# Kernel optimization log

Hardware: AMD Instinct MI355X
Metric: run time of the kernel (lower is better)

## Reference

```python
import jax, jax.numpy as jnp
import numpy as np

BLOCK_SIZE = 1024
DILATIONS = (1, 2, 4, 8)


def setup_inputs() -> dict:
    key = jax.random.key(0)
    kq, kk, kv, kw, kb = jax.random.split(key, 5)
    b, h, L, hd = 4, 8, 4096, 64
    hidden = h * hd
    return {
        "query_states": jax.random.normal(kq, (b, h, L, hd), jnp.float32),
        "key_states": jax.random.normal(kk, (b, h, L, hd), jnp.float32),
        "value_states": jax.random.normal(kv, (b, h, L, hd), jnp.float32),
        "Wo": jax.random.normal(kw, (hidden, hidden), jnp.float32),
        "bo": jax.random.normal(kb, (hidden,), jnp.float32),
    }


def _dilated_branch(q, k, v, d):
    """One dilation pass: strided gather -> block attention.
    Returns de (bsz, nh, Ld, 1) detached exp-row-sums and a (bsz, nh, Ld, hd)."""
    b, h, L, hd = q.shape
    qs, ks, vs = q[:, :, ::d], k[:, :, ::d], v[:, :, ::d]
    Ld = qs.shape[2]
    bs = min(BLOCK_SIZE, Ld)          # torch.split: one short block if Ld < block_size
    nb = Ld // bs                      # even split for chosen q_len
    blk = lambda x: x.reshape(b, h, nb, bs, hd)
    qb, kb, vb = blk(qs), blk(ks), blk(vs)
    scores = jnp.einsum('bhnqd,bhnkd->bhnqk', qb, kb) / jnp.sqrt(jnp.float32(hd))
    # detached, unstabilized exp-sum (matches attn_weights.detach().exp().sum(-1))
    de = jax.lax.stop_gradient(jnp.exp(scores).sum(-1, keepdims=True)).reshape(b, h, Ld, 1)
    probs = jax.nn.softmax(scores.astype(jnp.float32), axis=-1).astype(q.dtype)
    a = jnp.einsum('bhnqk,bhnkd->bhnqd', probs, vb).reshape(b, h, Ld, hd)
    return de, a


def reference(query_states, key_states, value_states, Wo, bo):
    b, h, L, hd = query_states.shape
    w = jnp.zeros((b, h, L, 1), jnp.float32)
    des, rs = [], []
    for d in DILATIONS:
        de, a = _dilated_branch(query_states, key_states, value_states, d)
        des.append(de)
        rs.append(a)
        w = w.at[:, :, ::d].add(de)
    out = jnp.zeros_like(query_states)
    for d, de, a in zip(DILATIONS, des, rs):
        aw = de / w[:, :, ::d]                     # (b, h, Ld, 1) relative weight
        out = out.at[:, :, ::d].add((aw * a).astype(query_states.dtype))
    out = out.transpose(0, 2, 1, 3).reshape(b, L, h * hd)
    return out @ Wo.T + bo
```

## Files before the change

kernel.cpp:

```cpp
#include <hip/hip_runtime.h>
#include <hip/hip_bf16.h>

typedef __attribute__((ext_vector_type(8))) short bf16x8;
typedef __attribute__((ext_vector_type(4))) float f32x4;
typedef unsigned short u16;

union F8 { bf16x8 v; unsigned u[4]; u16 s[8]; uint4 q; };

__device__ __forceinline__ unsigned pk2(float a, float b) {
    __hip_bfloat162 t = __float22bfloat162_rn(make_float2(a, b));
    unsigned r; __builtin_memcpy(&r, &t, 4); return r;
}
__device__ __forceinline__ u16 f2bf(float a) {
    __hip_bfloat16 t = __float2bfloat16(a);
    u16 r; __builtin_memcpy(&r, &t, 2); return r;
}
__device__ __forceinline__ float bf2f(u16 s) {
    unsigned u = ((unsigned)s) << 16; float f; __builtin_memcpy(&f, &u, 4); return f;
}
#define SWZ(byteoff, row) ((byteoff) ^ (((row) & 7) << 4))
#define MFMA(a, b, c) __builtin_amdgcn_mfma_f32_16x16x32_bf16((a), (b), (c), 0, 0, 0)

__global__ __launch_bounds__(256)
void prep_kernel(const float* __restrict__ K, const float* __restrict__ V,
                 u16* __restrict__ Kb, u16* __restrict__ Vt)
{
    __shared__ __align__(16) char tl[64 * 128];
    int blk = blockIdx.x;
    const int t = threadIdx.x;

    if (blk < 2048) {
        const int bh = blk >> 6, qt = blk & 63;
        const int q = qt * 64 + (t >> 2), dd0 = (t & 3) * 16;
        const float* kp = K + ((size_t)bh * 4096 + q) * 64 + dd0;
        float4 x0 = ((const float4*)kp)[0], x1 = ((const float4*)kp)[1];
        float4 x2 = ((const float4*)kp)[2], x3 = ((const float4*)kp)[3];
        F8 f0, f1;
        f0.u[0] = pk2(x0.x, x0.y); f0.u[1] = pk2(x0.z, x0.w);
        f0.u[2] = pk2(x1.x, x1.y); f0.u[3] = pk2(x1.z, x1.w);
        f1.u[0] = pk2(x2.x, x2.y); f1.u[1] = pk2(x2.z, x2.w);
        f1.u[2] = pk2(x3.x, x3.y); f1.u[3] = pk2(x3.z, x3.w);
        u16* op = Kb + ((size_t)bh * 4096 + q) * 64 + dd0;
        ((uint4*)op)[0] = f0.q; ((uint4*)op)[1] = f1.q;
        return;
    }
    blk -= 2048;
    int d, Ld; size_t vtoff;
    if (blk < 2048)      { d = 1; Ld = 4096; vtoff = 0; }
    else if (blk < 3072) { blk -= 2048; d = 2; Ld = 2048; vtoff = 8388608; }
    else if (blk < 3584) { blk -= 3072; d = 4; Ld = 1024; vtoff = 12582912; }
    else                 { blk -= 3584; d = 8; Ld = 512;  vtoff = 14680064; }
    const int tpb = Ld >> 6;
    const int bh = blk / tpb, jt = blk % tpb;
    {
        const int j = t >> 2, dd0 = (t & 3) * 16;
        const int q = (jt * 64 + j) * d;
        const float* vp = V + ((size_t)bh * 4096 + q) * 64 + dd0;
        float4 x0 = ((const float4*)vp)[0], x1 = ((const float4*)vp)[1];
        float4 x2 = ((const float4*)vp)[2], x3 = ((const float4*)vp)[3];
        F8 f0, f1;
        f0.u[0] = pk2(x0.x, x0.y); f0.u[1] = pk2(x0.z, x0.w);
        f0.u[2] = pk2(x1.x, x1.y); f0.u[3] = pk2(x1.z, x1.w);
        f1.u[0] = pk2(x2.x, x2.y); f1.u[1] = pk2(x2.z, x2.w);
        f1.u[2] = pk2(x3.x, x3.y); f1.u[3] = pk2(x3.z, x3.w);
        *(uint4*)(tl + SWZ(j * 128 + dd0 * 2, j)) = f0.q;
        *(uint4*)(tl + SWZ(j * 128 + dd0 * 2 + 16, j)) = f1.q;
    }
    __syncthreads();
    {
        const int dd = t >> 2, jb = (t & 3) * 16;
        F8 f0, f1;
#pragma unroll
        for (int i = 0; i < 8; ++i) {
            f0.s[i] = *(const u16*)(tl + SWZ((jb + i) * 128 + dd * 2, jb + i));
            f1.s[i] = *(const u16*)(tl + SWZ((jb + 8 + i) * 128 + dd * 2, jb + 8 + i));
        }
        u16* op = Vt + vtoff + ((size_t)bh * 64 + dd) * Ld + jt * 64 + jb;
        ((uint4*)op)[0] = f0.q; ((uint4*)op)[1] = f1.q;
    }
}

__global__ __launch_bounds__(256)
void attn_mfma(const float* __restrict__ Q, const u16* __restrict__ Kb,
               const u16* __restrict__ Vt, float* __restrict__ num,
               float* __restrict__ wsum, int d, int bs, int npb, int first,
               size_t vtoff)
{
    const int L = 4096;
    const int per = gridDim.x >> 3;
    const int wg0 = blockIdx.x;
    const int wg = (wg0 & 7) * per + (wg0 >> 3);

    const int bh = wg / npb;
    const int qt = wg % npb;
    const int b = bh >> 3, h = bh & 7;
    const int tid = threadIdx.x;
    const int w = tid >> 6, lane = tid & 63;
    const int g = lane >> 4, c = lane & 15;
    const int bstart = ((qt * 128) / bs) * bs;
    const int qrow0 = qt * 128 + w * 32;
    const int Ld = npb * 128;

    __shared__ __align__(16) char smem[32 * 1024];
    char* const Kls = smem;
    char* const Vls = smem + 8192;
    char* const Pls = smem + 16384 + w * 4096;

    const size_t base = (size_t)bh * L * 64;
    const size_t vbase = vtoff + (size_t)bh * 64 * Ld;
    const float qs = 0.125f * 1.44269504088896341f;

    bf16x8 qf[2][2];
#pragma unroll
    for (int qi = 0; qi < 2; ++qi) {
        const float* qp = Q + base + (size_t)(qrow0 + qi * 16 + c) * d * 64 + g * 8;
#pragma unroll
        for (int s = 0; s < 2; ++s) {
            float4 x = ((const float4*)(qp + s * 32))[0];
            float4 y = ((const float4*)(qp + s * 32))[1];
            F8 f;
            f.u[0] = pk2(x.x * qs, x.y * qs);
            f.u[1] = pk2(x.z * qs, x.w * qs);
            f.u[2] = pk2(y.x * qs, y.y * qs);
            f.u[3] = pk2(y.z * qs, y.w * qs);
            qf[qi][s] = f.v;
        }
    }

    f32x4 o[2][4];
#pragma unroll
    for (int qi = 0; qi < 2; ++qi)
#pragma unroll
        for (int dj = 0; dj < 4; ++dj) o[qi][dj] = (f32x4){0.f, 0.f, 0.f, 0.f};
    float lrow[2] = {0.f, 0.f};

    const int krow = tid >> 2, kc = tid & 3;

    uint4 ka, kb2, va, vb;
    {
        const u16* kp = Kb + base + (size_t)(bstart + krow) * d * 64 + kc * 16;
        ka = ((const uint4*)kp)[0]; kb2 = ((const uint4*)kp)[1];
        const u16* vp = Vt + vbase + (size_t)lane * Ld + bstart + w * 16;
        va = ((const uint4*)vp)[0]; vb = ((const uint4*)vp)[1];
    }

    for (int kt = 0; kt < bs; kt += 64) {
        *(uint4*)(Kls + SWZ(krow * 128 + kc * 32, krow)) = ka;
        *(uint4*)(Kls + SWZ(krow * 128 + kc * 32 + 16, krow)) = kb2;
        *(uint4*)(Vls + SWZ(lane * 128 + w * 32, lane)) = va;
        *(uint4*)(Vls + SWZ(lane * 128 + w * 32 + 16, lane)) = vb;
        __syncthreads();

        if (kt + 64 < bs) {
            const u16* kp = Kb + base + (size_t)(bstart + kt + 64 + krow) * d * 64 + kc * 16;
            ka = ((const uint4*)kp)[0]; kb2 = ((const uint4*)kp)[1];
            const u16* vp = Vt + vbase + (size_t)lane * Ld + bstart + kt + 64 + w * 16;
            va = ((const uint4*)vp)[0]; vb = ((const uint4*)vp)[1];
        }

        f32x4 st[2][4];
#pragma unroll
        for (int kj = 0; kj < 4; ++kj) {
            const int row = 16 * kj + c;
            bf16x8 kf0 = *(const bf16x8*)(Kls + SWZ(row * 128 + g * 16, row));
            bf16x8 kf1 = *(const bf16x8*)(Kls + SWZ(row * 128 + 64 + g * 16, row));
            f32x4 z = (f32x4){0.f, 0.f, 0.f, 0.f};
            st[0][kj] = MFMA(kf1, qf[0][1], MFMA(kf0, qf[0][0], z));
            st[1][kj] = MFMA(kf1, qf[1][1], MFMA(kf0, qf[1][0], z));
        }

#pragma unroll
        for (int qi = 0; qi < 2; ++qi) {
            const int prow = 16 * qi + c;
            float rs = 0.f;
#pragma unroll
            for (int kj = 0; kj < 4; ++kj) {
                const float p0 = exp2f(st[qi][kj][0]);
                const float p1 = exp2f(st[qi][kj][1]);
                const float p2 = exp2f(st[qi][kj][2]);
                const float p3 = exp2f(st[qi][kj][3]);
                rs += (p0 + p1) + (p2 + p3);
                uint2 pv; pv.x = pk2(p0, p1); pv.y = pk2(p2, p3);
                *(uint2*)(Pls + SWZ(prow * 128 + kj * 32 + g * 8, prow)) = pv;
            }
            lrow[qi] += rs;
        }

#pragma unroll
        for (int s = 0; s < 2; ++s) {
            bf16x8 vf[4], pf[2];
#pragma unroll
            for (int dj = 0; dj < 4; ++dj) {
                const int row = 16 * dj + c;
                vf[dj] = *(const bf16x8*)(Vls + SWZ(row * 128 + s * 64 + g * 16, row));
            }
#pragma unroll
            for (int qi = 0; qi < 2; ++qi) {
                const int row = 16 * qi + c;
                pf[qi] = *(const bf16x8*)(Pls + SWZ(row * 128 + s * 64 + g * 16, row));
            }
#pragma unroll
            for (int qi = 0; qi < 2; ++qi)
#pragma unroll
                for (int dj = 0; dj < 4; ++dj)
                    o[qi][dj] = MFMA(pf[qi], vf[dj], o[qi][dj]);
        }
        __syncthreads();
    }

#pragma unroll
    for (int qi = 0; qi < 2; ++qi) {
        float lq = lrow[qi];
        lq += __shfl_xor(lq, 16);
        lq += __shfl_xor(lq, 32);
#pragma unroll
        for (int r = 0; r < 4; ++r) {
            const int q = qrow0 + 16 * qi + 4 * g + r;
            float* np = num + ((size_t)b * L + (size_t)q * d) * 512 + h * 64 + c;
            if (first) {
#pragma unroll
                for (int dj = 0; dj < 4; ++dj) np[dj * 16] = o[qi][dj][r];
            } else {
#pragma unroll
                for (int dj = 0; dj < 4; ++dj) np[dj * 16] += o[qi][dj][r];
            }
        }
        if (g == 0) {
            const int q2 = qrow0 + 16 * qi + c;
            const size_t wi = ((size_t)b * L + (size_t)q2 * d) * 8 + h;
            if (first) wsum[wi] = lq;
            else       wsum[wi] += lq;
        }
    }
}

__global__ __launch_bounds__(256)
void proj_mfma(const float* __restrict__ num, const float* __restrict__ wsum,
               const float* __restrict__ Wo, const float* __restrict__ bo,
               float* __restrict__ out)
{
    __shared__ __align__(16) char smem[64 * 1024];
    char* const Ah = smem;
    char* const Al = smem + 16384;
    char* const Bh = smem + 32768;
    char* const Bl = smem + 49152;

    const int tid = threadIdx.x;
    const int w = tid >> 6, lane = tid & 63, g = lane >> 4, c = lane & 15;
    const int wm = (w >> 1) * 64, wn = (w & 1) * 64;
    const int per = gridDim.x >> 3;
    const int wg0 = blockIdx.x;
    const int wg = (wg0 & 7) * per + (wg0 >> 3);
    const int bm = (wg >> 2) * 128, bn = (wg & 3) * 128;
    const int srow = tid >> 1, koff = (tid & 1) * 32;

    f32x4 acc[4][4];
#pragma unroll
    for (int mi = 0; mi < 4; ++mi)
#pragma unroll
        for (int ni = 0; ni < 4; ++ni) acc[mi][ni] = (f32x4){0.f, 0.f, 0.f, 0.f};

    for (int bk = 0; bk < 512; bk += 64) {
        {
            const float* ap = num + (size_t)(bm + srow) * 512 + bk + koff;
            const float winv = 1.0f / wsum[(size_t)(bm + srow) * 8 + (bk >> 6)];
#pragma unroll
            for (int i = 0; i < 8; ++i) {
                float4 a4 = ((const float4*)ap)[i];
                float v0 = a4.x * winv, v1 = a4.y * winv, v2 = a4.z * winv, v3 = a4.w * winv;
                u16 h0 = f2bf(v0), h1 = f2bf(v1), h2 = f2bf(v2), h3 = f2bf(v3);
                uint2 hi; hi.x = h0 | ((unsigned)h1 << 16); hi.y = h2 | ((unsigned)h3 << 16);
                uint2 lo;
                lo.x = f2bf(v0 - bf2f(h0)) | ((unsigned)f2bf(v1 - bf2f(h1)) << 16);
                lo.y = f2bf(v2 - bf2f(h2)) | ((unsigned)f2bf(v3 - bf2f(h3)) << 16);
                const int off = SWZ(srow * 128 + koff * 2 + i * 8, srow);
                *(uint2*)(Ah + off) = hi;
                *(uint2*)(Al + off) = lo;
            }
            const float* bp = Wo + (size_t)(bn + srow) * 512 + bk + koff;
#pragma unroll
            for (int i = 0; i < 8; ++i) {
                float4 a4 = ((const float4*)bp)[i];
                u16 h0 = f2bf(a4.x), h1 = f2bf(a4.y), h2 = f2bf(a4.z), h3 = f2bf(a4.w);
                uint2 hi; hi.x = h0 | ((unsigned)h1 << 16); hi.y = h2 | ((unsigned)h3 << 16);
                uint2 lo;
                lo.x = f2bf(a4.x - bf2f(h0)) | ((unsigned)f2bf(a4.y - bf2f(h1)) << 16);
                lo.y = f2bf(a4.z - bf2f(h2)) | ((unsigned)f2bf(a4.w - bf2f(h3)) << 16);
                const int off = SWZ(srow * 128 + koff * 2 + i * 8, srow);
                *(uint2*)(Bh + off) = hi;
                *(uint2*)(Bl + off) = lo;
            }
        }
        __syncthreads();
#pragma unroll
        for (int s = 0; s < 2; ++s) {
            bf16x8 ah[4], al[4], bh[4], bl[4];
#pragma unroll
            for (int mi = 0; mi < 4; ++mi) {
                const int row = wm + 16 * mi + c;
                const int off = SWZ(row * 128 + s * 64 + g * 16, row);
                ah[mi] = *(const bf16x8*)(Ah + off);
                al[mi] = *(const bf16x8*)(Al + off);
            }
#pragma unroll
            for (int ni = 0; ni < 4; ++ni) {
                const int row = wn + 16 * ni + c;
                const int off = SWZ(row * 128 + s * 64 + g * 16, row);
                bh[ni] = *(const bf16x8*)(Bh + off);
                bl[ni] = *(const bf16x8*)(Bl + off);
            }
#pragma unroll
            for (int mi = 0; mi < 4; ++mi)
#pragma unroll
                for (int ni = 0; ni < 4; ++ni) {
                    acc[mi][ni] = MFMA(ah[mi], bh[ni], acc[mi][ni]);
                    acc[mi][ni] = MFMA(ah[mi], bl[ni], acc[mi][ni]);
                    acc[mi][ni] = MFMA(al[mi], bh[ni], acc[mi][ni]);
                }
        }
        __syncthreads();
    }

    float bias[4];
#pragma unroll
    for (int ni = 0; ni < 4; ++ni) bias[ni] = bo[bn + wn + 16 * ni + c];
#pragma unroll
    for (int mi = 0; mi < 4; ++mi)
#pragma unroll
        for (int r = 0; r < 4; ++r) {
            float* op = out + (size_t)(bm + wm + 16 * mi + 4 * g + r) * 512 + bn + wn + c;
#pragma unroll
            for (int ni = 0; ni < 4; ++ni)
                op[ni * 16] = acc[mi][ni][r] + bias[ni];
        }
}

extern "C" void kernel_launch(void* const* d_in, const int* in_sizes, int n_in,
                              void* d_out, int out_size, void* d_ws, size_t ws_size,
                              hipStream_t stream)
{
    const float* Q  = (const float*)d_in[0];
    const float* K  = (const float*)d_in[1];
    const float* V  = (const float*)d_in[2];
    const float* Wo = (const float*)d_in[3];
    const float* bo = (const float*)d_in[4];
    float* out = (float*)d_out;

    float* num  = (float*)d_ws;
    float* wsum = num + (size_t)8388608;
    u16*  Kb    = (u16*)((char*)d_ws + 34078720);
    u16*  Vt    = (u16*)((char*)d_ws + 50855936);
    const size_t vtoffs[4] = {0, 8388608, 12582912, 14680064};

    hipLaunchKernelGGL(prep_kernel, dim3(5888), dim3(256), 0, stream, K, V, Kb, Vt);

    const int dil[4] = {1, 2, 4, 8};
    for (int i = 0; i < 4; ++i) {
        const int d  = dil[i];
        const int Ld = 4096 / d;
        const int bs = (Ld < 1024) ? Ld : 1024;
        const int npb = Ld / 128;
        hipLaunchKernelGGL(attn_mfma, dim3(32 * npb), dim3(256), 0, stream,
                           Q, Kb, Vt, num, wsum, d, bs, npb, (i == 0) ? 1 : 0,
                           vtoffs[i]);
    }
    hipLaunchKernelGGL(proj_mfma, dim3(512), dim3(256), 0, stream,
                       num, wsum, Wo, bo, out);
}
```

Before: 224.0 us.

## Fuse four dilation attention launches into one grid with atomic accumulation

Replaces the four per-dilation attention launches with a single 1920-workgroup launch in which each workgroup derives its dilation, block size and offsets from its index. Because branches now run concurrently, the numerator and weight-sum outputs are accumulated with float atomicAdd into a buffer zeroed by a memset. This removes launch gaps and the tail effects of the small later launches, at the cost of atomic traffic, an extra 34MB memset, and nondeterministic summation order.

```diff
diff --git a/kernel.cpp b/kernel.cpp
--- a/kernel.cpp
+++ b/kernel.cpp
@@ -81,18 +81,23 @@
 }
 
 __global__ __launch_bounds__(256)
-void attn_mfma(const float* __restrict__ Q, const u16* __restrict__ Kb,
-               const u16* __restrict__ Vt, float* __restrict__ num,
-               float* __restrict__ wsum, int d, int bs, int npb, int first,
-               size_t vtoff)
+void attn_fused(const float* __restrict__ Q, const u16* __restrict__ Kb,
+                const u16* __restrict__ Vt, float* __restrict__ num,
+                float* __restrict__ wsum)
 {
     const int L = 4096;
     const int per = gridDim.x >> 3;
     const int wg0 = blockIdx.x;
     const int wg = (wg0 & 7) * per + (wg0 >> 3);
 
-    const int bh = wg / npb;
-    const int qt = wg % npb;
+    int d, npb, bs, rel; size_t vtoff;
+    if (wg < 1024)      { d = 1; npb = 32; bs = 1024; rel = wg;        vtoff = 0; }
+    else if (wg < 1536) { d = 2; npb = 16; bs = 1024; rel = wg - 1024; vtoff = 8388608; }
+    else if (wg < 1792) { d = 4; npb = 8;  bs = 1024; rel = wg - 1536; vtoff = 12582912; }
+    else                { d = 8; npb = 4;  bs = 512;  rel = wg - 1792; vtoff = 14680064; }
+
+    const int bh = rel / npb;
+    const int qt = rel % npb;
     const int b = bh >> 3, h = bh & 7;
     const int tid = threadIdx.x;
     const int w = tid >> 6, lane = tid & 63;
@@ -217,19 +222,13 @@
         for (int r = 0; r < 4; ++r) {
             const int q = qrow0 + 16 * qi + 4 * g + r;
             float* np = num + ((size_t)b * L + (size_t)q * d) * 512 + h * 64 + c;
-            if (first) {
-#pragma unroll
-                for (int dj = 0; dj < 4; ++dj) np[dj * 16] = o[qi][dj][r];
-            } else {
-#pragma unroll
-                for (int dj = 0; dj < 4; ++dj) np[dj * 16] += o[qi][dj][r];
-            }
+#pragma unroll
+            for (int dj = 0; dj < 4; ++dj)
+                atomicAdd(np + dj * 16, o[qi][dj][r]);
         }
         if (g == 0) {
             const int q2 = qrow0 + 16 * qi + c;
-            const size_t wi = ((size_t)b * L + (size_t)q2 * d) * 8 + h;
-            if (first) wsum[wi] = lq;
-            else       wsum[wi] += lq;
+            atomicAdd(wsum + ((size_t)b * L + (size_t)q2 * d) * 8 + h, lq);
         }
     }
 }
@@ -350,20 +349,12 @@
     float* wsum = num + (size_t)8388608;
     u16*  Kb    = (u16*)((char*)d_ws + 34078720);
     u16*  Vt    = (u16*)((char*)d_ws + 50855936);
-    const size_t vtoffs[4] = {0, 8388608, 12582912, 14680064};
+
+    hipMemsetAsync(d_ws, 0, 34078720, stream);
 
     hipLaunchKernelGGL(prep_kernel, dim3(5888), dim3(256), 0, stream, K, V, Kb, Vt);
-
-    const int dil[4] = {1, 2, 4, 8};
-    for (int i = 0; i < 4; ++i) {
-        const int d  = dil[i];
-        const int Ld = 4096 / d;
-        const int bs = (Ld < 1024) ? Ld : 1024;
-        const int npb = Ld / 128;
-        hipLaunchKernelGGL(attn_mfma, dim3(32 * npb), dim3(256), 0, stream,
-                           Q, Kb, Vt, num, wsum, d, bs, npb, (i == 0) ? 1 : 0,
-                           vtoffs[i]);
-    }
+    hipLaunchKernelGGL(attn_fused, dim3(1920), dim3(256), 0, stream,
+                       Q, Kb, Vt, num, wsum);
     hipLaunchKernelGGL(proj_mfma, dim3(512), dim3(256), 0, stream,
                        num, wsum, Wo, bo, out);
 }
```

Result: faster. 217.5 us (-2.9%).
